# Kernel tuning notes

Measured on AMD Instinct MI355X. Metric: run time of the kernel, lower is better.

## Reference

```python
import jax, jax.numpy as jnp
import numpy as np

N_EMB = 1024
HEAD = 64
BLOCK = 2048
BATCH = 8


def setup_inputs() -> dict:
    key = jax.random.key(0)
    k_in, k_q, k_k, k_v = jax.random.split(key, 4)
    inp = jax.random.normal(k_in, (BATCH, BLOCK, N_EMB), dtype=jnp.float32)
    s = 1.0 / np.sqrt(N_EMB)
    Wq = jax.random.uniform(k_q, (N_EMB, HEAD), dtype=jnp.float32, minval=-s, maxval=s)
    Wk = jax.random.uniform(k_k, (N_EMB, HEAD), dtype=jnp.float32, minval=-s, maxval=s)
    Wv = jax.random.uniform(k_v, (N_EMB, HEAD), dtype=jnp.float32, minval=-s, maxval=s)
    return {"input": inp, "Wq": Wq, "Wk": Wk, "Wv": Wv}


def reference(input, Wq, Wk, Wv):
    # input: [B, T, E]; projections to head_size H
    q = jnp.einsum('bte,eh->bth', input, Wq)
    k = jnp.einsum('bte,eh->bth', input, Wk)
    v = jnp.einsum('bte,eh->bth', input, Wv)
    scale = 1.0 / np.sqrt(HEAD).astype(np.float32)
    # [B, T, T] causal scores
    scores = jnp.einsum('bqh,bkh->bqk', q, k) * scale
    T = input.shape[1]
    causal = jnp.tril(jnp.ones((T, T), dtype=bool))
    scores = jnp.where(causal, scores, jnp.float32(-jnp.inf))
    wei = jax.nn.softmax(scores, axis=-1)
    # dropout is identity in eval mode (p=0.1 omitted for deterministic reference)
    return jnp.einsum('bqk,bkh->bqh', wei, v)
```

## Files before the change

kernel.cpp:

```cpp
#include <hip/hip_runtime.h>
#include <hip/hip_bf16.h>
#include <math.h>

#define BATCH 8
#define SEQ   2048
#define EMB   1024
#define HEAD  64
#define BT    (BATCH * SEQ)

typedef __attribute__((ext_vector_type(8))) short  short8;
typedef __attribute__((ext_vector_type(4))) short  short4v;
typedef __attribute__((ext_vector_type(4))) float  floatx4;

__device__ __forceinline__ unsigned short f2bf(float x) {
    union { __hip_bfloat16 h; unsigned short u; } cv;
    cv.h = __float2bfloat16(x);
    return cv.u;
}

__device__ __forceinline__ void block_sync_lds() {
    asm volatile("s_waitcnt lgkmcnt(0)" ::: "memory");
    __builtin_amdgcn_s_barrier();
}

__global__ __launch_bounds__(256) void wt_prep(
    const float* __restrict__ Wq, const float* __restrict__ Wk,
    const float* __restrict__ Wv, unsigned short* __restrict__ WT)
{
    __shared__ float tile[64][65];
    const int w  = blockIdx.x >> 4;
    const int k0 = (blockIdx.x & 15) * 64;
    const float* W = (w == 0) ? Wq : (w == 1) ? Wk : Wv;
    const int tid = threadIdx.x;

    for (int idx = tid; idx < 4096; idx += 256) {
        const int kr = idx >> 6, n = idx & 63;
        tile[kr][n] = W[(size_t)(k0 + kr) * HEAD + n];
    }
    __syncthreads();
    const int n  = tid >> 2;
    const int k8 = (tid & 3) * 16;
    unsigned short* dst = WT + (size_t)(w * 64 + n) * EMB + k0 + k8;
    short8 v0, v1;
#pragma unroll
    for (int j = 0; j < 8; ++j) v0[j] = (short)f2bf(tile[k8 + j][n]);
#pragma unroll
    for (int j = 0; j < 8; ++j) v1[j] = (short)f2bf(tile[k8 + 8 + j][n]);
    *(short8*)(dst)     = v0;
    *(short8*)(dst + 8) = v1;
}

__global__ __launch_bounds__(512) void qkv_mfma(
    const float* __restrict__ X, const unsigned short* __restrict__ WT,
    unsigned short* __restrict__ Q, unsigned short* __restrict__ K,
    unsigned short* __restrict__ VT)
{
    __shared__ unsigned short Xs[2][32 * 64];

    const int tid = threadIdx.x;
    const int l   = tid & 63;
    const int wv  = tid >> 6;
    const int wm  = wv >> 2, wn = wv & 3;
    const int g   = l >> 4,  q  = l & 15;
    const int row0 = blockIdx.x * 32;

    const int sr = tid >> 4, sj = tid & 15;
    const float* xsrc = X + (size_t)(row0 + sr) * EMB + sj * 4;
    const int soff = sr * 128 + ((sj * 8) ^ ((sr & 7) << 4));
    char* const sdst0 = (char*)&Xs[0][0] + soff;
    char* const sdst1 = (char*)&Xs[1][0] + soff;

    const int rr  = wm * 16 + q;
    const int rsw = (rr & 7) << 4;
    const char* const rbase0 = (const char*)&Xs[0][0] + rr * 128;
    const char* const rbase1 = (const char*)&Xs[1][0] + rr * 128;

    const unsigned short* wbase = WT + (size_t)(wn * 48 + q) * EMB + g * 8;

    floatx4 acc[3];
#pragma unroll
    for (int nt = 0; nt < 3; ++nt) acc[nt] = (floatx4){0.f, 0.f, 0.f, 0.f};

    float4 xreg[2];
    short8 wreg[2][6];

    xreg[0] = *(const float4*)(xsrc);
    xreg[1] = *(const float4*)(xsrc + 64);
#pragma unroll
    for (int nt = 0; nt < 3; ++nt)
#pragma unroll
        for (int kc = 0; kc < 2; ++kc)
            wreg[0][nt * 2 + kc] = *(const short8*)(wbase + (size_t)nt * 16 * EMB + kc * 32);
    {
        const float4 xc = xreg[0];
        short4v b;
        b[0] = (short)f2bf(xc.x); b[1] = (short)f2bf(xc.y);
        b[2] = (short)f2bf(xc.z); b[3] = (short)f2bf(xc.w);
        *(short4v*)sdst0 = b;
    }

#pragma unroll
    for (int t = 0; t < 16; ++t) {
        if (t + 2 < 16)
            xreg[t & 1] = *(const float4*)(xsrc + (t + 2) * 64);
        if (t + 1 < 16) {
#pragma unroll
            for (int nt = 0; nt < 3; ++nt)
#pragma unroll
                for (int kc = 0; kc < 2; ++kc)
                    wreg[(t + 1) & 1][nt * 2 + kc] =
                        *(const short8*)(wbase + (size_t)nt * 16 * EMB + (t + 1) * 64 + kc * 32);
            const float4 xc = xreg[(t + 1) & 1];
            short4v b;
            b[0] = (short)f2bf(xc.x); b[1] = (short)f2bf(xc.y);
            b[2] = (short)f2bf(xc.z); b[3] = (short)f2bf(xc.w);
            block_sync_lds();
            *(short4v*)(((t + 1) & 1) ? sdst1 : sdst0) = b;
            block_sync_lds();
        }
#pragma unroll
        for (int kc = 0; kc < 2; ++kc) {
            const short8 a = *(const short8*)(((t & 1) ? rbase1 : rbase0)
                                              + ((kc * 64 + g * 16) ^ rsw));
#pragma unroll
            for (int nt = 0; nt < 3; ++nt)
                acc[nt] = __builtin_amdgcn_mfma_f32_16x16x32_bf16(
                    a, wreg[t & 1][nt * 2 + kc], acc[nt], 0, 0, 0);
        }
    }

    const int trow0 = row0 + wm * 16 + g * 4;
#pragma unroll
    for (int nt = 0; nt < 3; ++nt) {
        const int c = wn * 48 + nt * 16 + q;
#pragma unroll
        for (int r = 0; r < 4; ++r) {
            const unsigned short v = f2bf(acc[nt][r]);
            const int t = trow0 + r;
            if (c < 64) {
                Q[(size_t)t * HEAD + c] = v;
            } else if (c < 128) {
                K[(size_t)t * HEAD + (c - 64)] = v;
            } else {
                const int bb = t >> 11, tl = t & (SEQ - 1);
                VT[((size_t)bb * HEAD + (c - 128)) * SEQ + tl] = v;
            }
        }
    }
}

__global__ __launch_bounds__(256) void attn_mfma(
    const unsigned short* __restrict__ Q, const unsigned short* __restrict__ K,
    const unsigned short* __restrict__ VT, float* __restrict__ O)
{
    __shared__ unsigned short Ks[2][64][72];
    __shared__ unsigned short Vs[2][64][72];
    __shared__ unsigned short Ps[64][72];
    __shared__ float Mo[2][16][68];
    __shared__ float Mm[2][16], Ml[2][16];

    const int tid  = threadIdx.x;
    const int l    = tid & 63;
    const int wv   = tid >> 6;
    const int pair = wv >> 1, sub = wv & 1;
    const int g    = l >> 4, q = l & 15;
    const int qt   = 63 - (blockIdx.x >> 3);
    const int b    = blockIdx.x & 7;
    const int qrow0 = qt * 32 + sub * 16;
    const size_t kbase = (size_t)b * SEQ * HEAD;
    const size_t vbase = (size_t)b * HEAD * SEQ;

    short8 bq[2];
#pragma unroll
    for (int dc = 0; dc < 2; ++dc)
        bq[dc] = *(const short8*)&Q[kbase + (size_t)(qrow0 + q) * HEAD + dc * 32 + g * 8];

    floatx4 o[4];
#pragma unroll
    for (int dt = 0; dt < 4; ++dt) o[dt] = (floatx4){0.f, 0.f, 0.f, 0.f};
    float m_run = -INFINITY, l_run = 0.f;

    const int nkt = (qt >> 1) + 1;

    short8 kreg[2], vreg[2];
#pragma unroll
    for (int i = 0; i < 2; ++i) {
        const int c = tid + i * 256, r = c >> 3, k8 = (c & 7) * 8;
        kreg[i] = *(const short8*)&K [kbase + (size_t)r * HEAD + k8];
        vreg[i] = *(const short8*)&VT[vbase + (size_t)r * SEQ  + k8];
    }

    for (int kt = 0; kt < nkt; ++kt) {
        const int bs = kt & 1;
#pragma unroll
        for (int i = 0; i < 2; ++i) {
            const int c = tid + i * 256, r = c >> 3, k8 = (c & 7) * 8;
            *(short8*)&Ks[bs][r][k8] = kreg[i];
            *(short8*)&Vs[bs][r][k8] = vreg[i];
        }
        block_sync_lds();

        if (kt + 1 < nkt) {
#pragma unroll
            for (int i = 0; i < 2; ++i) {
                const int c = tid + i * 256, r = c >> 3, k8 = (c & 7) * 8;
                kreg[i] = *(const short8*)&K [kbase + (size_t)((kt + 1) * 64 + r) * HEAD + k8];
                vreg[i] = *(const short8*)&VT[vbase + (size_t)r * SEQ + (kt + 1) * 64 + k8];
            }
        }

        if ((kt & 1) == pair) {
            floatx4 s[4];
#pragma unroll
            for (int t = 0; t < 4; ++t) {
                s[t] = (floatx4){0.f, 0.f, 0.f, 0.f};
#pragma unroll
                for (int dc = 0; dc < 2; ++dc) {
                    const short8 ak = *(const short8*)&Ks[bs][t * 16 + q][dc * 32 + g * 8];
                    s[t] = __builtin_amdgcn_mfma_f32_16x16x32_bf16(ak, bq[dc], s[t], 0, 0, 0);
                }
            }

            float sv[4][4];
            if (kt == nkt - 1) {
#pragma unroll
                for (int t = 0; t < 4; ++t)
#pragma unroll
                    for (int r = 0; r < 4; ++r) {
                        const int kg = kt * 64 + t * 16 + g * 4 + r;
                        sv[t][r] = (kg > qrow0 + q) ? -INFINITY : s[t][r] * 0.125f;
                    }
            } else {
#pragma unroll
                for (int t = 0; t < 4; ++t)
#pragma unroll
                    for (int r = 0; r < 4; ++r) sv[t][r] = s[t][r] * 0.125f;
            }

            float pm = -INFINITY;
#pragma unroll
            for (int t = 0; t < 4; ++t)
#pragma unroll
                for (int r = 0; r < 4; ++r) pm = fmaxf(pm, sv[t][r]);
            pm = fmaxf(pm, __shfl_xor(pm, 16));
            pm = fmaxf(pm, __shfl_xor(pm, 32));
            const float mnew = fmaxf(m_run, pm);
            const float crow = __expf(m_run - mnew);
            float p[4][4];
            float psum = 0.f;
#pragma unroll
            for (int t = 0; t < 4; ++t)
#pragma unroll
                for (int r = 0; r < 4; ++r) {
                    p[t][r] = __expf(sv[t][r] - mnew);
                    psum += p[t][r];
                }
            psum += __shfl_xor(psum, 16);
            psum += __shfl_xor(psum, 32);
            l_run = l_run * crow + psum;
            m_run = mnew;

#pragma unroll
            for (int r = 0; r < 4; ++r) {
                const float cr = __shfl(crow, g * 4 + r);
#pragma unroll
                for (int dt = 0; dt < 4; ++dt) o[dt][r] *= cr;
            }

#pragma unroll
            for (int t = 0; t < 4; ++t) {
                const unsigned int lo = (unsigned)f2bf(p[t][0]) | ((unsigned)f2bf(p[t][1]) << 16);
                const unsigned int hi = (unsigned)f2bf(p[t][2]) | ((unsigned)f2bf(p[t][3]) << 16);
                *(unsigned int*)&Ps[wv * 16 + q][t * 16 + g * 4]     = lo;
                *(unsigned int*)&Ps[wv * 16 + q][t * 16 + g * 4 + 2] = hi;
            }
            asm volatile("s_waitcnt lgkmcnt(0)" ::: "memory");
            __builtin_amdgcn_sched_barrier(0);

#pragma unroll
            for (int kc = 0; kc < 2; ++kc) {
                const short8 pa = *(const short8*)&Ps[wv * 16 + q][kc * 32 + g * 8];
#pragma unroll
                for (int dt = 0; dt < 4; ++dt) {
                    const short8 vb = *(const short8*)&Vs[bs][dt * 16 + q][kc * 32 + g * 8];
                    o[dt] = __builtin_amdgcn_mfma_f32_16x16x32_bf16(pa, vb, o[dt], 0, 0, 0);
                }
            }
        }
    }

    __syncthreads();
    if (pair == 1) {
#pragma unroll
        for (int dt = 0; dt < 4; ++dt)
#pragma unroll
            for (int r = 0; r < 4; ++r)
                Mo[sub][g * 4 + r][dt * 16 + q] = o[dt][r];
        if (g == 0) { Mm[sub][q] = m_run; Ml[sub][q] = l_run; }
    }
    __syncthreads();
    if (pair == 0) {
        const float m1  = Mm[sub][q];
        const float l1v = Ml[sub][q];
        const float mx  = fmaxf(m_run, m1);
        const float c0  = __expf(m_run - mx);
        const float c1  = __expf(m1 - mx);
        const float lm  = l_run * c0 + l1v * c1;
        const size_t obase = (size_t)b * SEQ * HEAD;
#pragma unroll
        for (int r = 0; r < 4; ++r) {
            const float c0r = __shfl(c0, g * 4 + r);
            const float c1r = __shfl(c1, g * 4 + r);
            const float lr  = __shfl(lm, g * 4 + r);
            const float inv = 1.0f / lr;
#pragma unroll
            for (int dt = 0; dt < 4; ++dt) {
                const float val = o[dt][r] * c0r + Mo[sub][g * 4 + r][dt * 16 + q] * c1r;
                O[obase + (size_t)(qrow0 + g * 4 + r) * HEAD + dt * 16 + q] = val * inv;
            }
        }
    }
}

extern "C" void kernel_launch(void* const* d_in, const int* in_sizes, int n_in,
                              void* d_out, int out_size, void* d_ws, size_t ws_size,
                              hipStream_t stream)
{
    const float* X  = (const float*)d_in[0];
    const float* Wq = (const float*)d_in[1];
    const float* Wk = (const float*)d_in[2];
    const float* Wv = (const float*)d_in[3];
    float* O = (float*)d_out;

    unsigned short* Qb = (unsigned short*)d_ws;
    unsigned short* Kb = Qb + (size_t)BT * HEAD;
    unsigned short* Vt = Kb + (size_t)BT * HEAD;
    unsigned short* WT = Vt + (size_t)BT * HEAD;

    wt_prep  <<<dim3(48),  dim3(256), 0, stream>>>(Wq, Wk, Wv, WT);
    qkv_mfma <<<dim3(512), dim3(512), 0, stream>>>(X, WT, Qb, Kb, Vt);
    attn_mfma<<<dim3(512), dim3(256), 0, stream>>>(Qb, Kb, Vt, O);
}
```

Measured before the change: 171.3 us.

## Load full X row-block into LDS once and read K/V fragments directly from global

The QKV projection now loads the whole 32x1024 X tile into LDS up front, converting it to bf16 with a single barrier. This replaces the per-K-step double-buffered staging that needed two barriers per step. The attention kernel drops the shared K/V tiles and block-wide barriers. Each wave pair now loads its own K and V MFMA fragments straight from global memory, with K prefetched one iteration ahead, and iterates only over its own key tiles. This removes LDS staging and synchronisation, at the cost of a 64KB LDS footprint in the projection kernel, which limits occupancy, and of uncoalesced, redundant global loads in attention that depend on the cache.

```diff
diff --git a/kernel.cpp b/kernel.cpp
--- a/kernel.cpp
+++ b/kernel.cpp
@@ -55,7 +55,7 @@
     unsigned short* __restrict__ Q, unsigned short* __restrict__ K,
     unsigned short* __restrict__ VT)
 {
-    __shared__ unsigned short Xs[2][32 * 64];
+    __shared__ unsigned short Xs[32 * 1024];
 
     const int tid = threadIdx.x;
     const int l   = tid & 63;
@@ -66,43 +66,40 @@
 
     const int sr = tid >> 4, sj = tid & 15;
     const float* xsrc = X + (size_t)(row0 + sr) * EMB + sj * 4;
-    const int soff = sr * 128 + ((sj * 8) ^ ((sr & 7) << 4));
-    char* const sdst0 = (char*)&Xs[0][0] + soff;
-    char* const sdst1 = (char*)&Xs[1][0] + soff;
+    char* const sbase = (char*)Xs + sr * 2048;
+    const int ssw = (sr & 7) << 4;
+
+    float4 xr[16];
+#pragma unroll
+    for (int i = 0; i < 16; ++i) xr[i] = *(const float4*)(xsrc + i * 64);
+
+    const unsigned short* wbase = WT + (size_t)(wn * 48 + q) * EMB + g * 8;
+    short8 wreg[2][6];
+#pragma unroll
+    for (int nt = 0; nt < 3; ++nt)
+#pragma unroll
+        for (int kc = 0; kc < 2; ++kc)
+            wreg[0][nt * 2 + kc] = *(const short8*)(wbase + (size_t)nt * 16 * EMB + kc * 32);
+
+#pragma unroll
+    for (int i = 0; i < 16; ++i) {
+        short4v bb;
+        bb[0] = (short)f2bf(xr[i].x); bb[1] = (short)f2bf(xr[i].y);
+        bb[2] = (short)f2bf(xr[i].z); bb[3] = (short)f2bf(xr[i].w);
+        *(short4v*)(sbase + ((sj * 8 + i * 128) ^ ssw)) = bb;
+    }
+    block_sync_lds();
 
     const int rr  = wm * 16 + q;
     const int rsw = (rr & 7) << 4;
-    const char* const rbase0 = (const char*)&Xs[0][0] + rr * 128;
-    const char* const rbase1 = (const char*)&Xs[1][0] + rr * 128;
-
-    const unsigned short* wbase = WT + (size_t)(wn * 48 + q) * EMB + g * 8;
+    const char* const rbase = (const char*)Xs + rr * 2048;
 
     floatx4 acc[3];
 #pragma unroll
     for (int nt = 0; nt < 3; ++nt) acc[nt] = (floatx4){0.f, 0.f, 0.f, 0.f};
 
-    float4 xreg[2];
-    short8 wreg[2][6];
-
-    xreg[0] = *(const float4*)(xsrc);
-    xreg[1] = *(const float4*)(xsrc + 64);
-#pragma unroll
-    for (int nt = 0; nt < 3; ++nt)
-#pragma unroll
-        for (int kc = 0; kc < 2; ++kc)
-            wreg[0][nt * 2 + kc] = *(const short8*)(wbase + (size_t)nt * 16 * EMB + kc * 32);
-    {
-        const float4 xc = xreg[0];
-        short4v b;
-        b[0] = (short)f2bf(xc.x); b[1] = (short)f2bf(xc.y);
-        b[2] = (short)f2bf(xc.z); b[3] = (short)f2bf(xc.w);
-        *(short4v*)sdst0 = b;
-    }
-
 #pragma unroll
     for (int t = 0; t < 16; ++t) {
-        if (t + 2 < 16)
-            xreg[t & 1] = *(const float4*)(xsrc + (t + 2) * 64);
         if (t + 1 < 16) {
 #pragma unroll
             for (int nt = 0; nt < 3; ++nt)
@@ -110,18 +107,10 @@
                 for (int kc = 0; kc < 2; ++kc)
                     wreg[(t + 1) & 1][nt * 2 + kc] =
                         *(const short8*)(wbase + (size_t)nt * 16 * EMB + (t + 1) * 64 + kc * 32);
-            const float4 xc = xreg[(t + 1) & 1];
-            short4v b;
-            b[0] = (short)f2bf(xc.x); b[1] = (short)f2bf(xc.y);
-            b[2] = (short)f2bf(xc.z); b[3] = (short)f2bf(xc.w);
-            block_sync_lds();
-            *(short4v*)(((t + 1) & 1) ? sdst1 : sdst0) = b;
-            block_sync_lds();
         }
 #pragma unroll
         for (int kc = 0; kc < 2; ++kc) {
-            const short8 a = *(const short8*)(((t & 1) ? rbase1 : rbase0)
-                                              + ((kc * 64 + g * 16) ^ rsw));
+            const short8 a = *(const short8*)(rbase + ((t * 128 + kc * 64 + g * 16) ^ rsw));
 #pragma unroll
             for (int nt = 0; nt < 3; ++nt)
                 acc[nt] = __builtin_amdgcn_mfma_f32_16x16x32_bf16(
@@ -153,8 +142,6 @@
     const unsigned short* __restrict__ Q, const unsigned short* __restrict__ K,
     const unsigned short* __restrict__ VT, float* __restrict__ O)
 {
-    __shared__ unsigned short Ks[2][64][72];
-    __shared__ unsigned short Vs[2][64][72];
     __shared__ unsigned short Ps[64][72];
     __shared__ float Mo[2][16][68];
     __shared__ float Mm[2][16], Ml[2][16];
@@ -182,110 +169,104 @@
 
     const int nkt = (qt >> 1) + 1;
 
-    short8 kreg[2], vreg[2];
-#pragma unroll
-    for (int i = 0; i < 2; ++i) {
-        const int c = tid + i * 256, r = c >> 3, k8 = (c & 7) * 8;
-        kreg[i] = *(const short8*)&K [kbase + (size_t)r * HEAD + k8];
-        vreg[i] = *(const short8*)&VT[vbase + (size_t)r * SEQ  + k8];
-    }
-
-    for (int kt = 0; kt < nkt; ++kt) {
-        const int bs = kt & 1;
-#pragma unroll
-        for (int i = 0; i < 2; ++i) {
-            const int c = tid + i * 256, r = c >> 3, k8 = (c & 7) * 8;
-            *(short8*)&Ks[bs][r][k8] = kreg[i];
-            *(short8*)&Vs[bs][r][k8] = vreg[i];
-        }
-        block_sync_lds();
-
-        if (kt + 1 < nkt) {
-#pragma unroll
-            for (int i = 0; i < 2; ++i) {
-                const int c = tid + i * 256, r = c >> 3, k8 = (c & 7) * 8;
-                kreg[i] = *(const short8*)&K [kbase + (size_t)((kt + 1) * 64 + r) * HEAD + k8];
-                vreg[i] = *(const short8*)&VT[vbase + (size_t)r * SEQ + (kt + 1) * 64 + k8];
+    short8 kf[4][2];
+#pragma unroll
+    for (int t = 0; t < 4; ++t)
+#pragma unroll
+        for (int dc = 0; dc < 2; ++dc)
+            kf[t][dc] = *(const short8*)&K[kbase
+                + (size_t)(pair * 64 + t * 16 + q) * HEAD + dc * 32 + g * 8];
+
+    for (int kt = pair; kt < nkt; kt += 2) {
+        floatx4 s[4];
+#pragma unroll
+        for (int t = 0; t < 4; ++t) {
+            s[t] = (floatx4){0.f, 0.f, 0.f, 0.f};
+#pragma unroll
+            for (int dc = 0; dc < 2; ++dc)
+                s[t] = __builtin_amdgcn_mfma_f32_16x16x32_bf16(kf[t][dc], bq[dc], s[t], 0, 0, 0);
+        }
+
+        short8 vf[2][4];
+#pragma unroll
+        for (int kc = 0; kc < 2; ++kc)
+#pragma unroll
+            for (int dt = 0; dt < 4; ++dt)
+                vf[kc][dt] = *(const short8*)&VT[vbase
+                    + (size_t)(dt * 16 + q) * SEQ + kt * 64 + kc * 32 + g * 8];
+
+        {
+            const int ktn = (kt + 2 < nkt) ? (kt + 2) : 0;
+#pragma unroll
+            for (int t = 0; t < 4; ++t)
+#pragma unroll
+                for (int dc = 0; dc < 2; ++dc)
+                    kf[t][dc] = *(const short8*)&K[kbase
+                        + (size_t)(ktn * 64 + t * 16 + q) * HEAD + dc * 32 + g * 8];
+        }
+
+        float sv[4][4];
+        if (kt == nkt - 1) {
+#pragma unroll
+            for (int t = 0; t < 4; ++t)
+#pragma unroll
+                for (int r = 0; r < 4; ++r) {
+                    const int kg = kt * 64 + t * 16 + g * 4 + r;
+                    sv[t][r] = (kg > qrow0 + q) ? -INFINITY : s[t][r] * 0.125f;
+                }
+        } else {
+#pragma unroll
+            for (int t = 0; t < 4; ++t)
+#pragma unroll
+                for (int r = 0; r < 4; ++r) sv[t][r] = s[t][r] * 0.125f;
+        }
+
+        float pm = -INFINITY;
+#pragma unroll
+        for (int t = 0; t < 4; ++t)
+#pragma unroll
+            for (int r = 0; r < 4; ++r) pm = fmaxf(pm, sv[t][r]);
+        pm = fmaxf(pm, __shfl_xor(pm, 16));
+        pm = fmaxf(pm, __shfl_xor(pm, 32));
+        const float mnew = fmaxf(m_run, pm);
+        const float crow = __expf(m_run - mnew);
+        float p[4][4];
+        float psum = 0.f;
+#pragma unroll
+        for (int t = 0; t < 4; ++t)
+#pragma unroll
+            for (int r = 0; r < 4; ++r) {
+                p[t][r] = __expf(sv[t][r] - mnew);
+                psum += p[t][r];
             }
-        }
-
-        if ((kt & 1) == pair) {
-            floatx4 s[4];
-#pragma unroll
-            for (int t = 0; t < 4; ++t) {
-                s[t] = (floatx4){0.f, 0.f, 0.f, 0.f};
-#pragma unroll
-                for (int dc = 0; dc < 2; ++dc) {
-                    const short8 ak = *(const short8*)&Ks[bs][t * 16 + q][dc * 32 + g * 8];
-                    s[t] = __builtin_amdgcn_mfma_f32_16x16x32_bf16(ak, bq[dc], s[t], 0, 0, 0);
-                }
-            }
-
-            float sv[4][4];
-            if (kt == nkt - 1) {
-#pragma unroll
-                for (int t = 0; t < 4; ++t)
-#pragma unroll
-                    for (int r = 0; r < 4; ++r) {
-                        const int kg = kt * 64 + t * 16 + g * 4 + r;
-                        sv[t][r] = (kg > qrow0 + q) ? -INFINITY : s[t][r] * 0.125f;
-                    }
-            } else {
-#pragma unroll
-                for (int t = 0; t < 4; ++t)
-#pragma unroll
-                    for (int r = 0; r < 4; ++r) sv[t][r] = s[t][r] * 0.125f;
-            }
-
-            float pm = -INFINITY;
-#pragma unroll
-            for (int t = 0; t < 4; ++t)
-#pragma unroll
-                for (int r = 0; r < 4; ++r) pm = fmaxf(pm, sv[t][r]);
-            pm = fmaxf(pm, __shfl_xor(pm, 16));
-            pm = fmaxf(pm, __shfl_xor(pm, 32));
-            const float mnew = fmaxf(m_run, pm);
-            const float crow = __expf(m_run - mnew);
-            float p[4][4];
-            float psum = 0.f;
-#pragma unroll
-            for (int t = 0; t < 4; ++t)
-#pragma unroll
-                for (int r = 0; r < 4; ++r) {
-                    p[t][r] = __expf(sv[t][r] - mnew);
-                    psum += p[t][r];
-                }
-            psum += __shfl_xor(psum, 16);
-            psum += __shfl_xor(psum, 32);
-            l_run = l_run * crow + psum;
-            m_run = mnew;
-
-#pragma unroll
-            for (int r = 0; r < 4; ++r) {
-                const float cr = __shfl(crow, g * 4 + r);
-#pragma unroll
-                for (int dt = 0; dt < 4; ++dt) o[dt][r] *= cr;
-            }
-
-#pragma unroll
-            for (int t = 0; t < 4; ++t) {
-                const unsigned int lo = (unsigned)f2bf(p[t][0]) | ((unsigned)f2bf(p[t][1]) << 16);
-                const unsigned int hi = (unsigned)f2bf(p[t][2]) | ((unsigned)f2bf(p[t][3]) << 16);
-                *(unsigned int*)&Ps[wv * 16 + q][t * 16 + g * 4]     = lo;
-                *(unsigned int*)&Ps[wv * 16 + q][t * 16 + g * 4 + 2] = hi;
-            }
-            asm volatile("s_waitcnt lgkmcnt(0)" ::: "memory");
-            __builtin_amdgcn_sched_barrier(0);
-
-#pragma unroll
-            for (int kc = 0; kc < 2; ++kc) {
-                const short8 pa = *(const short8*)&Ps[wv * 16 + q][kc * 32 + g * 8];
-#pragma unroll
-                for (int dt = 0; dt < 4; ++dt) {
-                    const short8 vb = *(const short8*)&Vs[bs][dt * 16 + q][kc * 32 + g * 8];
-                    o[dt] = __builtin_amdgcn_mfma_f32_16x16x32_bf16(pa, vb, o[dt], 0, 0, 0);
-                }
-            }
+        psum += __shfl_xor(psum, 16);
+        psum += __shfl_xor(psum, 32);
+        l_run = l_run * crow + psum;
+        m_run = mnew;
+
+#pragma unroll
+        for (int r = 0; r < 4; ++r) {
+            const float cr = __shfl(crow, g * 4 + r);
+#pragma unroll
+            for (int dt = 0; dt < 4; ++dt) o[dt][r] *= cr;
+        }
+
+#pragma unroll
+        for (int t = 0; t < 4; ++t) {
+            const unsigned int lo = (unsigned)f2bf(p[t][0]) | ((unsigned)f2bf(p[t][1]) << 16);
+            const unsigned int hi = (unsigned)f2bf(p[t][2]) | ((unsigned)f2bf(p[t][3]) << 16);
+            *(unsigned int*)&Ps[wv * 16 + q][t * 16 + g * 4]     = lo;
+            *(unsigned int*)&Ps[wv * 16 + q][t * 16 + g * 4 + 2] = hi;
+        }
+        asm volatile("s_waitcnt lgkmcnt(0)" ::: "memory");
+        __builtin_amdgcn_sched_barrier(0);
+
+#pragma unroll
+        for (int kc = 0; kc < 2; ++kc) {
+            const short8 pa = *(const short8*)&Ps[wv * 16 + q][kc * 32 + g * 8];
+#pragma unroll
+            for (int dt = 0; dt < 4; ++dt)
+                o[dt] = __builtin_amdgcn_mfma_f32_16x16x32_bf16(pa, vf[kc][dt], o[dt], 0, 0, 0);
         }
     }
 
```

Measured after the change: 184.4 us. +7.7%, slower.
